# Kernel optimization log

Measured on AMD Instinct MI355X. Metric: run time of the kernel, lower is better.

The kernel has to match this reference:

```python
import math
import jax, jax.numpy as jnp
import numpy as np

B, S, D, H, FF, E, V, RH = 8, 256, 512, 8, 2048, 8, 32000, 256
MAX_PATH, MAX_VISITS = 4, 2
NEG = -1e9
DH = D // H


def _make_pe():
    # PositionalEncoding buffer (sin/cos), sliced to seq len S
    pos = np.arange(S, dtype=np.float32)[:, None]
    div = np.exp(np.arange(0, D, 2, dtype=np.float32) * (-math.log(10000.0) / D))
    pe = np.zeros((S, D), dtype=np.float32)
    pe[:, 0::2] = np.sin(pos * div)
    pe[:, 1::2] = np.cos(pos * div)
    return jnp.asarray(pe[None])  # [1,S,D]


def setup_inputs() -> dict:
    key = jax.random.key(0)
    ks = jax.random.split(key, 12)
    s = 0.02
    return dict(
        input_ids=jax.random.randint(ks[0], (B, S), 0, V),
        emb=jax.random.normal(ks[1], (V, D), jnp.float32) * s,
        pe=_make_pe(),
        Wqkv=jax.random.normal(ks[2], (E, 3 * D, D), jnp.float32) * s,
        bqkv=jnp.zeros((E, 3 * D), jnp.float32),
        Wo=jax.random.normal(ks[3], (E, D, D), jnp.float32) * s,
        bo=jnp.zeros((E, D), jnp.float32),
        W1=jax.random.normal(ks[4], (E, FF, D), jnp.float32) * s,
        b1=jnp.zeros((E, FF), jnp.float32),
        W2=jax.random.normal(ks[5], (E, D, FF), jnp.float32) * s,
        b2=jnp.zeros((E, D), jnp.float32),
        ln1_g=jnp.ones((E, D), jnp.float32), ln1_b=jnp.zeros((E, D), jnp.float32),
        ln2_g=jnp.ones((E, D), jnp.float32), ln2_b=jnp.zeros((E, D), jnp.float32),
        tag=jax.random.normal(ks[6], (E, D), jnp.float32) * 0.01,
        r_w1=jax.random.normal(ks[7], (RH, D), jnp.float32) * s,
        r_b1=jnp.zeros((RH,), jnp.float32),
        r_w2=jax.random.normal(ks[8], (E + 1, RH), jnp.float32) * s,
        r_b2=jnp.zeros((E + 1,), jnp.float32),
        lm_w=jax.random.normal(ks[9], (V, D), jnp.float32) * s,
        lm_b=jnp.zeros((V,), jnp.float32),
    )


def _ln(x, g, b):
    # per-sample gathered LayerNorm params g,b: [B,D]; x: [B,S,D]
    mu = x.mean(-1, keepdims=True)
    var = ((x - mu) ** 2).mean(-1, keepdims=True)
    return (x - mu) * jax.lax.rsqrt(var + 1e-5) * g[:, None, :] + b[:, None, :]


def _expert(x, idx, Wqkv, bqkv, Wo, bo, W1, b1, W2, b2, g1, be1, g2, be2, tag):
    # post-norm TransformerEncoderLayer (eval mode, dropout off) with per-sample expert params
    qkv = jnp.einsum('bsd,bfd->bsf', x, Wqkv[idx]) + bqkv[idx][:, None, :]
    q, k, v = jnp.split(qkv, 3, axis=-1)
    q = q.reshape(B, S, H, DH)
    k = k.reshape(B, S, H, DH)
    v = v.reshape(B, S, H, DH)
    att = jax.nn.softmax(jnp.einsum('bqhd,bkhd->bhqk', q, k) / math.sqrt(DH), axis=-1)
    ctx = jnp.einsum('bhqk,bkhd->bqhd', att, v).reshape(B, S, D)
    attn_out = jnp.einsum('bsd,bod->bso', ctx, Wo[idx]) + bo[idx][:, None, :]
    x = _ln(x + attn_out, g1[idx], be1[idx])
    hid = jax.nn.relu(jnp.einsum('bsd,bfd->bsf', x, W1[idx]) + b1[idx][:, None, :])
    ff = jnp.einsum('bsf,bdf->bsd', hid, W2[idx]) + b2[idx][:, None, :]
    x = _ln(x + ff, g2[idx], be2[idx])
    return x + tag[idx][:, None, :]  # + specialization_tag


def reference(input_ids, emb, pe, Wqkv, bqkv, Wo, bo, W1, b1, W2, b2,
              ln1_g, ln1_b, ln2_g, ln2_b, tag, r_w1, r_b1, r_w2, r_b2, lm_w, lm_b):
    pad_mask = (jnp.arange(V) != 0).astype(emb.dtype)[:, None]  # padding_idx=0 row is zero
    rep = (emb * pad_mask)[input_ids] * math.sqrt(D) + pe[:, :S]
    visits = jnp.zeros((B, E), jnp.int32)
    active = jnp.ones((B,), bool)
    ent_total = jnp.asarray(0.0, rep.dtype)
    for _ in range(MAX_PATH):
        summary = rep.mean(1)  # [B,D]
        h = jax.nn.relu(summary @ r_w1.T + r_b1)
        logits = h @ r_w2.T + r_b2  # [B,E+1], last slot = terminate
        logits = jnp.concatenate(
            [jnp.where(visits >= MAX_VISITS, NEG, logits[:, :E]), logits[:, E:]], axis=1)
        probs = jax.nn.softmax(logits, axis=-1)
        ent = -jnp.sum(probs * jnp.log(probs + 1e-9), axis=-1)
        cnt = jnp.sum(active)
        ent_total = ent_total + jnp.where(
            cnt > 0, jnp.sum(ent * active) / jnp.maximum(cnt, 1).astype(ent.dtype), 0.0)
        choice = jnp.argmax(logits, axis=-1)       # eval mode: hard argmax
        go = active & (choice < E)                 # samples routed to an expert this step
        idx = jnp.where(go, choice, 0)
        visits = visits + jax.nn.one_hot(idx, E, dtype=jnp.int32) * go[:, None].astype(jnp.int32)
        new_rep = _expert(rep, idx, Wqkv, bqkv, Wo, bo, W1, b1, W2, b2,
                          ln1_g, ln1_b, ln2_g, ln2_b, tag)
        rep = jnp.where(go[:, None, None], new_rep, rep)  # terminated/inactive reps frozen
        active = go
    logits_lm = rep @ lm_w.T + lm_b  # [B,S,V]
    return logits_lm, ent_total
```

## Files before the change

### kernel.cpp

```cpp
#include <hip/hip_runtime.h>
#include <hip/hip_bf16.h>

#define NB 8
#define NS 256
#define ND 512
#define NH 8
#define NDH 64
#define NFF 2048
#define NE 8
#define NV 32000
#define NRH 256
#define MAXV 2
#define NEGV (-1e9f)

typedef __attribute__((ext_vector_type(8))) short short8;
typedef __attribute__((ext_vector_type(4))) float f32x4;

__device__ __forceinline__ unsigned short f2bf(float x) {
  unsigned int u = __float_as_uint(x);
  u = (u + 0x7fffu + ((u >> 16) & 1u)) >> 16;
  return (unsigned short)u;
}

__device__ __forceinline__ void gload16(const unsigned short* g, unsigned short* l) {
  __builtin_amdgcn_global_load_lds(
      (const __attribute__((address_space(1))) unsigned int*)g,
      (__attribute__((address_space(3))) unsigned int*)l, 16, 0, 0);
}

__device__ __forceinline__ int swzc(int lane) {
  return (lane & 3) ^ ((lane >> 3) & 3);
}

__device__ __forceinline__ void cast8(const float* s, unsigned short* d, int j) {
  const float4* s4 = (const float4*)s;
  float4 a = s4[j * 2], b = s4[j * 2 + 1];
  short8 v;
  v[0] = (short)f2bf(a.x); v[1] = (short)f2bf(a.y);
  v[2] = (short)f2bf(a.z); v[3] = (short)f2bf(a.w);
  v[4] = (short)f2bf(b.x); v[5] = (short)f2bf(b.y);
  v[6] = (short)f2bf(b.z); v[7] = (short)f2bf(b.w);
  *(short8*)&d[(size_t)j * 8] = v;
}

__global__ __launch_bounds__(256) void k_cast5e(
    const float* s0, unsigned short* d0, int n0,
    const float* s1, unsigned short* d1, int n1,
    const float* s2, unsigned short* d2, int n2,
    const float* s3, unsigned short* d3, int n3,
    const float* s4, unsigned short* d4, int n4,
    int nbcast,
    const int* __restrict__ ids, const float* __restrict__ emb,
    const float* __restrict__ pe, float* __restrict__ rep,
    unsigned short* __restrict__ repb, float* __restrict__ partial,
    int* visits, int* active, float* entp) {
  if (blockIdx.x == 0) {
    if (threadIdx.x < NB * NE) visits[threadIdx.x] = 0;
    if (threadIdx.x < NB) active[threadIdx.x] = 1;
    if (threadIdx.x == 0) *entp = 0.f;
  }
  if ((int)blockIdx.x >= nbcast) {
    int j2 = blockIdx.x - nbcast;
    int rg = j2 & 15, b = j2 >> 4;
    int t = threadIdx.x;
    int c0 = t, c1 = t + 256;
    float p0 = 0.f, p1 = 0.f;
    for (int row = 0; row < 16; ++row) {
      int s = rg * 16 + row;
      int id = ids[b * NS + s];
      float sc = (id != 0) ? 22.627416997969522f : 0.f;
      float v0 = emb[(size_t)id * ND + c0] * sc + pe[(size_t)s * ND + c0];
      float v1 = emb[(size_t)id * ND + c1] * sc + pe[(size_t)s * ND + c1];
      size_t base = ((size_t)b * NS + s) * ND;
      rep[base + c0] = v0; rep[base + c1] = v1;
      repb[base + c0] = f2bf(v0); repb[base + c1] = f2bf(v1);
      p0 += v0; p1 += v1;
    }
    float* pp = partial + ((size_t)b * 16 + rg) * ND;
    pp[c0] = p0; pp[c1] = p1;
    return;
  }
  int j = blockIdx.x * 256 + threadIdx.x;
  if (j < n0) { cast8(s0, d0, j); return; }
  j -= n0;
  if (j < n1) { cast8(s1, d1, j); return; }
  j -= n1;
  if (j < n2) { cast8(s2, d2, j); return; }
  j -= n2;
  if (j < n3) { cast8(s3, d3, j); return; }
  j -= n3;
  if (j < n4) cast8(s4, d4, j);
}

__global__ __launch_bounds__(256) void k_router(const float* __restrict__ partial,
                                                const float* __restrict__ rw1,
                                                const float* __restrict__ rb1,
                                                const float* __restrict__ rw2,
                                                const float* __restrict__ rb2,
                                                int* visits, int* active,
                                                int* idx, int* go, float* ent_total) {
  __shared__ float sm[NB][ND];
  __shared__ float h[NB][NRH];
  __shared__ float lg[NB][NE + 1];
  int t = threadIdx.x;
  for (int i = t; i < NB * ND; i += 256) {
    int bb = i >> 9, d = i & 511;
    const float* pp = partial + ((size_t)bb * 16) * ND + d;
    float s = 0.f;
#pragma unroll
    for (int rg = 0; rg < 16; ++rg) s += pp[(size_t)rg * ND];
    sm[bb][d] = s * (1.f / NS);
  }
  __syncthreads();
  {
    const float* w = rw1 + (size_t)t * ND;
    float acc[NB];
#pragma unroll
    for (int b = 0; b < NB; ++b) acc[b] = rb1[t];
    for (int d = 0; d < ND; ++d) {
      float wv = w[d];
#pragma unroll
      for (int b = 0; b < NB; ++b) acc[b] += sm[b][d] * wv;
    }
#pragma unroll
    for (int b = 0; b < NB; ++b) h[b][t] = fmaxf(acc[b], 0.f);
  }
  __syncthreads();
  if (t < NB * (NE + 1)) {
    int b = t / (NE + 1), e = t % (NE + 1);
    const float* w = rw2 + e * NRH;
    float a = rb2[e];
    for (int r = 0; r < NRH; ++r) a += h[b][r] * w[r];
    lg[b][e] = a;
  }
  __syncthreads();
  if (t == 0) {
    int aprev[NB];
    int cnt = 0;
    for (int b = 0; b < NB; ++b) { aprev[b] = active[b]; cnt += aprev[b]; }
    float entsum = 0.f;
    for (int b = 0; b < NB; ++b) {
      float l[NE + 1];
      for (int e = 0; e < NE; ++e)
        l[e] = (visits[b * NE + e] >= MAXV) ? NEGV : lg[b][e];
      l[NE] = lg[b][NE];
      float m = l[0];
      for (int e = 1; e <= NE; ++e) m = fmaxf(m, l[e]);
      float z = 0.f, p[NE + 1];
      for (int e = 0; e <= NE; ++e) { p[e] = __expf(l[e] - m); z += p[e]; }
      float zi = 1.f / z, ent = 0.f;
      for (int e = 0; e <= NE; ++e) {
        float pp = p[e] * zi;
        ent -= pp * __logf(pp + 1e-9f);
      }
      if (aprev[b]) entsum += ent;
      int ch = 0; float bm = l[0];
      for (int e = 1; e <= NE; ++e) if (l[e] > bm) { bm = l[e]; ch = e; }
      int g = (aprev[b] && ch < NE) ? 1 : 0;
      int ix = g ? ch : 0;
      visits[b * NE + ix] += g;
      idx[b] = ix; go[b] = g; active[b] = g;
    }
    if (cnt > 0) *ent_total += entsum / (float)cnt;
  }
}

template <int OUT, int RELU, int SK>
__global__ __launch_bounds__(256) void k_gemm64p(
    const unsigned short* __restrict__ Aall, int sa,
    const unsigned short* __restrict__ Wall, const float* __restrict__ ball,
    float* __restrict__ Pall, unsigned short* __restrict__ Uall, int so,
    int N, int K,
    unsigned short* __restrict__ Qb, unsigned short* __restrict__ Kb,
    unsigned short* __restrict__ Vt,
    const int* __restrict__ go, const int* __restrict__ idx) {
  int b = blockIdx.z;
  if (!go[b]) return;
  int t = threadIdx.x;
  int lane = t & 63, w = t >> 6;
  int wm = (w >> 1) * 32, wn = (w & 1) * 32;
  int kc = blockIdx.x >> 2;
  int bm = (blockIdx.x & 3) * 64, bn = blockIdx.y * 64;
  int KC = K / SK;
  int lrow = (lane >> 4) * 4, lcol = lane & 15;
  const unsigned short* A = Aall + (size_t)b * sa + kc * KC;
  const unsigned short* W = Wall + (size_t)idx[b] * N * K + kc * KC;

  __shared__ __align__(16) unsigned short As[2][64][64];
  __shared__ __align__(16) unsigned short Bs[2][64][64];
  f32x4 acc[2][2];
#pragma unroll
  for (int i = 0; i < 2; ++i)
#pragma unroll
    for (int j = 0; j < 2; ++j) acc[i][j] = (f32x4){0.f, 0.f, 0.f, 0.f};

  int ch8 = (lane & 7) ^ ((lane >> 3) & 7);
  const unsigned short* ga = A + (size_t)(bm + w * 16 + (lane >> 3)) * K + ch8 * 8;
  const unsigned short* gb = W + (size_t)(bn + w * 16 + (lane >> 3)) * K + ch8 * 8;

#define ISSUE64(slot, kt)                                            \
  gload16(ga + (size_t)(kt) * 64, &As[slot][w * 16][0]);             \
  gload16(ga + (size_t)(kt) * 64 + 8 * (size_t)K, &As[slot][w * 16 + 8][0]); \
  gload16(gb + (size_t)(kt) * 64, &Bs[slot][w * 16][0]);             \
  gload16(gb + (size_t)(kt) * 64 + 8 * (size_t)K, &Bs[slot][w * 16 + 8][0]);

  int nk = KC >> 6;
  ISSUE64(0, 0)
  ISSUE64(1, 1)

  int row0 = lane & 15, g = lane >> 4;
  for (int it = 0; it < nk; ++it) {
    if (it < nk - 1) asm volatile("s_waitcnt vmcnt(4)" ::: "memory");
    else             asm volatile("s_waitcnt vmcnt(0)" ::: "memory");
    asm volatile("s_barrier" ::: "memory");
    int sl = it & 1;
    __builtin_amdgcn_s_setprio(1);
#pragma unroll
    for (int kk = 0; kk < 2; ++kk) {
      int co = ((kk * 4 + g) ^ (row0 & 7)) * 8;
      short8 a0 = *(const short8*)&As[sl][wm + row0][co];
      short8 a1 = *(const short8*)&As[sl][wm + 16 + row0][co];
      short8 b0 = *(const short8*)&Bs[sl][wn + row0][co];
      short8 b1 = *(const short8*)&Bs[sl][wn + 16 + row0][co];
      acc[0][0] = __builtin_amdgcn_mfma_f32_16x16x32_bf16(a0, b0, acc[0][0], 0, 0, 0);
      acc[0][1] = __builtin_amdgcn_mfma_f32_16x16x32_bf16(a0, b1, acc[0][1], 0, 0, 0);
      acc[1][0] = __builtin_amdgcn_mfma_f32_16x16x32_bf16(a1, b0, acc[1][0], 0, 0, 0);
      acc[1][1] = __builtin_amdgcn_mfma_f32_16x16x32_bf16(a1, b1, acc[1][1], 0, 0, 0);
    }
    __builtin_amdgcn_s_setprio(0);
    asm volatile("s_barrier" ::: "memory");
    if (it + 2 < nk) { ISSUE64(sl, it + 2) }
  }
#undef ISSUE64

  if (OUT == 2) {
    const float* bias = ball + (size_t)idx[b] * N;
    int seg = bn >> 9;
#pragma unroll
    for (int nf = 0; nf < 2; ++nf) {
      int col = bn + wn + nf * 16 + lcol;
      float bv = bias[col];
      if (seg < 2) {
        unsigned short* dst = (seg == 0) ? Qb : Kb;
        int cc = col - seg * 512;
#pragma unroll
        for (int mf = 0; mf < 2; ++mf)
#pragma unroll
          for (int r = 0; r < 4; ++r) {
            int row = bm + wm + mf * 16 + lrow + r;
            dst[((size_t)b * NS + row) * ND + cc] = f2bf(acc[mf][nf][r] + bv);
          }
      } else {
        int dcol = col - 1024;
#pragma unroll
        for (int mf = 0; mf < 2; ++mf) {
          int s0 = bm + wm + mf * 16 + lrow;
          unsigned long long pk =
              (unsigned long long)f2bf(acc[mf][nf][0] + bv) |
              ((unsigned long long)f2bf(acc[mf][nf][1] + bv) << 16) |
              ((unsigned long long)f2bf(acc[mf][nf][2] + bv) << 32) |
              ((unsigned long long)f2bf(acc[mf][nf][3] + bv) << 48);
          *(unsigned long long*)&Vt[((size_t)b * 512 + dcol) * 256 + s0] = pk;
        }
      }
    }
  } else if (OUT == 1) {
    const float* bias = ball + (size_t)idx[b] * N;
#pragma unroll
    for (int nf = 0; nf < 2; ++nf) {
      int col = bn + wn + nf * 16 + lcol;
      float bv = bias[col];
#pragma unroll
      for (int mf = 0; mf < 2; ++mf) {
#pragma unroll
        for (int r = 0; r < 4; ++r) {
          int row = bm + wm + mf * 16 + lrow + r;
          float v = acc[mf][nf][r] + bv;
          if (RELU) v = fmaxf(v, 0.f);
          Uall[(size_t)b * so + (size_t)row * N + col] = f2bf(v);
        }
      }
    }
  } else {
    float* P = Pall + ((size_t)kc * NB + b) * ((size_t)NS * N);
#pragma unroll
    for (int nf = 0; nf < 2; ++nf) {
      int col = bn + wn + nf * 16 + lcol;
#pragma unroll
      for (int mf = 0; mf < 2; ++mf)
#pragma unroll
        for (int r = 0; r < 4; ++r)
          P[(size_t)(bm + wm + mf * 16 + lrow + r) * N + col] = acc[mf][nf][r];
    }
  }
}

__global__ __launch_bounds__(256) void k_attn2(const unsigned short* __restrict__ Qb,
                                               const unsigned short* __restrict__ Kb,
                                               const unsigned short* __restrict__ Vt,
                                               unsigned short* __restrict__ ctxb,
                                               const int* __restrict__ go) {
  int b = blockIdx.z, h = blockIdx.y, qt = blockIdx.x;
  if (!go[b]) return;
  int t = threadIdx.x;
  __shared__ __align__(16) unsigned short lds0[16384];
  __shared__ __align__(16) unsigned short lds1[16384];
  int lane = t & 63, w = t >> 6, g = lane >> 4, c = lane & 15;

#pragma unroll
  for (int i = 0; i < 8; ++i) {
    int task = i * 256 + t;
    int k = task >> 3, cc = task & 7;
    short8 v = *(const short8*)&Kb[((size_t)b * NS + k) * ND + h * NDH + cc * 8];
    *(short8*)&lds0[k * 64 + ((cc * 8) ^ ((k & 7) << 3))] = v;
  }
#pragma unroll
  for (int i = 0; i < 8; ++i) {
    int task = i * 256 + t;
    int d = task >> 5, kc = task & 31;
    short8 v = *(const short8*)&Vt[((size_t)b * 512 + h * NDH + d) * 256 + kc * 8];
    *(short8*)&lds1[d * 256 + ((kc * 8) ^ ((d & 7) << 3))] = v;
  }
  short8 qf[2];
  {
    const unsigned short* qp = Qb + ((size_t)b * NS + qt * 64 + w * 16 + c) * ND + h * NDH;
    qf[0] = *(const short8*)&qp[g * 8];
    qf[1] = *(const short8*)&qp[32 + g * 8];
  }
  __syncthreads();

  f32x4 sacc[16];
#pragma unroll
  for (int mf = 0; mf < 16; ++mf) sacc[mf] = (f32x4){0.f, 0.f, 0.f, 0.f};
#pragma unroll
  for (int mf = 0; mf < 16; ++mf) {
#pragma unroll
    for (int kd = 0; kd < 2; ++kd) {
      int row = mf * 16 + c;
      short8 kf = *(const short8*)&lds0[row * 64 + ((kd * 32 + g * 8) ^ ((row & 7) << 3))];
      sacc[mf] = __builtin_amdgcn_mfma_f32_16x16x32_bf16(kf, qf[kd], sacc[mf], 0, 0, 0);
    }
  }
  __syncthreads();

  float mx = -3.4e38f;
#pragma unroll
  for (int mf = 0; mf < 16; ++mf) {
#pragma unroll
    for (int r = 0; r < 4; ++r) {
      sacc[mf][r] *= 0.125f;
      mx = fmaxf(mx, sacc[mf][r]);
    }
  }
  mx = fmaxf(mx, __shfl_xor(mx, 16));
  mx = fmaxf(mx, __shfl_xor(mx, 32));
  float sum = 0.f;
#pragma unroll
  for (int mf = 0; mf < 16; ++mf)
#pragma unroll
    for (int r = 0; r < 4; ++r) {
      float p = __expf(sacc[mf][r] - mx);
      sacc[mf][r] = p;
      sum += p;
    }
  sum += __shfl_xor(sum, 16);
  sum += __shfl_xor(sum, 32);
  float zi = 1.f / sum;

  int q_l = w * 16 + c;
#pragma unroll
  for (int mf = 0; mf < 16; ++mf) {
    unsigned long long pk =
        (unsigned long long)f2bf(sacc[mf][0] * zi) |
        ((unsigned long long)f2bf(sacc[mf][1] * zi) << 16) |
        ((unsigned long long)f2bf(sacc[mf][2] * zi) << 32) |
        ((unsigned long long)f2bf(sacc[mf][3] * zi) << 48);
    *(unsigned long long*)&lds0[q_l * 256 + ((mf * 16 + g * 4) ^ ((q_l & 7) << 3))] = pk;
  }

  f32x4 cacc[4];
#pragma unroll
  for (int nf = 0; nf < 4; ++nf) cacc[nf] = (f32x4){0.f, 0.f, 0.f, 0.f};
#pragma unroll
  for (int ks = 0; ks < 8; ++ks) {
    int prow = w * 16 + c;
    short8 pf = *(const short8*)&lds0[prow * 256 + ((ks * 32 + g * 8) ^ ((prow & 7) << 3))];
#pragma unroll
    for (int nf = 0; nf < 4; ++nf) {
      int vrow = nf * 16 + c;
      short8 vf = *(const short8*)&lds1[vrow * 256 + ((ks * 32 + g * 8) ^ ((vrow & 7) << 3))];
      cacc[nf] = __builtin_amdgcn_mfma_f32_16x16x32_bf16(pf, vf, cacc[nf], 0, 0, 0);
    }
  }
#pragma unroll
  for (int nf = 0; nf < 4; ++nf)
#pragma unroll
    for (int r = 0; r < 4; ++r)
      ctxb[((size_t)b * NS + qt * 64 + w * 16 + g * 4 + r) * ND + h * NDH + nf * 16 + c] =
          f2bf(cacc[nf][r]);
}

template <int NCH, int TAG, int SUMP>
__global__ __launch_bounds__(256) void k_ln_red(
    const float* __restrict__ res, const float* __restrict__ part,
    const float* __restrict__ gbias,
    const float* __restrict__ gall, const float* __restrict__ beall,
    const float* __restrict__ tagall,
    float* __restrict__ outf, unsigned short* __restrict__ outb,
    float* __restrict__ sump,
    const int* __restrict__ go, const int* __restrict__ idx) {
  int b = blockIdx.y;
  if (!go[b]) return;
  int rg = blockIdx.x;
  int w = threadIdx.x >> 6, l = threadIdx.x & 63;
  int ix = idx[b];
  int d = l * 8;
  float gb8[8], gg[8], bb[8];
  {
    float4 a0 = *(const float4*)&gbias[ix * ND + d];
    float4 a1 = *(const float4*)&gbias[ix * ND + d + 4];
    gb8[0] = a0.x; gb8[1] = a0.y; gb8[2] = a0.z; gb8[3] = a0.w;
    gb8[4] = a1.x; gb8[5] = a1.y; gb8[6] = a1.z; gb8[7] = a1.w;
    float4 g0 = *(const float4*)&gall[ix * ND + d];
    float4 g1 = *(const float4*)&gall[ix * ND + d + 4];
    gg[0] = g0.x; gg[1] = g0.y; gg[2] = g0.z; gg[3] = g0.w;
    gg[4] = g1.x; gg[5] = g1.y; gg[6] = g1.z; gg[7] = g1.w;
    float4 b0 = *(const float4*)&beall[ix * ND + d];
    float4 b1 = *(const float4*)&beall[ix * ND + d + 4];
    bb[0] = b0.x; bb[1] = b0.y; bb[2] = b0.z; bb[3] = b0.w;
    bb[4] = b1.x; bb[5] = b1.y; bb[6] = b1.z; bb[7] = b1.w;
    if (TAG) {
      float4 t0 = *(const float4*)&tagall[ix * ND + d];
      float4 t1 = *(const float4*)&tagall[ix * ND + d + 4];
      bb[0] += t0.x; bb[1] += t0.y; bb[2] += t0.z; bb[3] += t0.w;
      bb[4] += t1.x; bb[5] += t1.y; bb[6] += t1.z; bb[7] += t1.w;
    }
  }
  float ps[8] = {0.f, 0.f, 0.f, 0.f, 0.f, 0.f, 0.f, 0.f};
  const size_t CSTRIDE = (size_t)NB * NS * ND;
  for (int rr = 0; rr < 4; ++rr) {
    int s = rg * 16 + w * 4 + rr;
    size_t base = ((size_t)b * NS + s) * ND;
    float4 x0 = *(const float4*)&res[base + d];
    float4 x1 = *(const float4*)&res[base + d + 4];
    float v[8] = {x0.x + gb8[0], x0.y + gb8[1], x0.z + gb8[2], x0.w + gb8[3],
                  x1.x + gb8[4], x1.y + gb8[5], x1.z + gb8[6], x1.w + gb8[7]};
#pragma unroll
    for (int c = 0; c < NCH; ++c) {
      const float* pc = part + c * CSTRIDE + base;
      float4 p0 = *(const float4*)&pc[d];
      float4 p1 = *(const float4*)&pc[d + 4];
      v[0] += p0.x; v[1] += p0.y; v[2] += p0.z; v[3] += p0.w;
      v[4] += p1.x; v[5] += p1.y; v[6] += p1.z; v[7] += p1.w;
    }
    float sum = 0.f;
#pragma unroll
    for (int j = 0; j < 8; ++j) sum += v[j];
#pragma unroll
    for (int off = 1; off < 64; off <<= 1) sum += __shfl_xor(sum, off);
    float mu = sum * (1.f / ND);
    float var = 0.f;
#pragma unroll
    for (int j = 0; j < 8; ++j) { v[j] -= mu; var += v[j] * v[j]; }
#pragma unroll
    for (int off = 1; off < 64; off <<= 1) var += __shfl_xor(var, off);
    float rs = rsqrtf(var * (1.f / ND) + 1e-5f);
    float o[8];
    short8 ob;
#pragma unroll
    for (int j = 0; j < 8; ++j) {
      o[j] = v[j] * rs * gg[j] + bb[j];
      if (SUMP) ps[j] += o[j];
      ob[j] = (short)f2bf(o[j]);
    }
    *(float4*)&outf[base + d] = (float4){o[0], o[1], o[2], o[3]};
    *(float4*)&outf[base + d + 4] = (float4){o[4], o[5], o[6], o[7]};
    *(short8*)&outb[base + d] = ob;
  }
  if (SUMP) {
    __shared__ float pl[4][ND];
#pragma unroll
    for (int j = 0; j < 8; ++j) pl[w][d + j] = ps[j];
    __syncthreads();
    if (w == 0) {
      float* pp = sump + ((size_t)b * 16 + rg) * ND;
#pragma unroll
      for (int j = 0; j < 8; ++j)
        pp[d + j] = pl[0][d + j] + pl[1][d + j] + pl[2][d + j] + pl[3][d + j];
    }
  }
}

__global__ __launch_bounds__(512, 2) void k_lmhead256(const unsigned short* __restrict__ Ab,
                                                      const unsigned short* __restrict__ Wb,
                                                      const float* __restrict__ bias,
                                                      float* __restrict__ out,
                                                      const float* __restrict__ entp) {
  if (blockIdx.x == 0 && threadIdx.x == 0)
    out[(size_t)NB * NS * NV] = *entp;
  int id = blockIdx.x;
  int swz = (id & 7) * 125 + (id >> 3);
  int bm = (swz % 8) * 256;
  int bn = (swz / 8) * 256;

  __shared__ __align__(16) unsigned short As[2][256][32];
  __shared__ __align__(16) unsigned short Bs[2][256][32];
  int t = threadIdx.x;
  int lane = t & 63, w = t >> 6;
  int wm = (w >> 2) * 128, wn = (w & 3) * 64;
  f32x4 acc[8][4];
#pragma unroll
  for (int i = 0; i < 8; ++i)
#pragma unroll
    for (int j = 0; j < 4; ++j) acc[i][j] = (f32x4){0.f, 0.f, 0.f, 0.f};

  const unsigned short* ga = Ab + (size_t)(bm + w * 32 + (lane >> 2)) * ND + swzc(lane) * 8;
  const unsigned short* gb = Wb + (size_t)(bn + w * 32 + (lane >> 2)) * ND + swzc(lane) * 8;

#define ISSUEL(slot, kt)                                           \
  gload16(ga + (kt) * 32, &As[slot][w * 32][0]);                   \
  gload16(ga + (kt) * 32 + 16 * ND, &As[slot][w * 32 + 16][0]);    \
  gload16(gb + (kt) * 32, &Bs[slot][w * 32][0]);                   \
  gload16(gb + (kt) * 32 + 16 * ND, &Bs[slot][w * 32 + 16][0]);

  ISSUEL(0, 0)
  ISSUEL(1, 1)

  int row0 = lane & 15;
  int cs = ((lane >> 4) ^ ((row0 >> 1) & 3)) * 8;
  for (int it = 0; it < 16; ++it) {
    if (it < 15) asm volatile("s_waitcnt vmcnt(4)" ::: "memory");
    else         asm volatile("s_waitcnt vmcnt(0)" ::: "memory");
    asm volatile("s_barrier" ::: "memory");
    int sl = it & 1;
    short8 a[8], bfr[4];
#pragma unroll
    for (int mf = 0; mf < 8; ++mf)
      a[mf] = *(const short8*)&As[sl][wm + mf * 16 + row0][cs];
#pragma unroll
    for (int nf = 0; nf < 4; ++nf)
      bfr[nf] = *(const short8*)&Bs[sl][wn + nf * 16 + row0][cs];
    __builtin_amdgcn_s_setprio(1);
#pragma unroll
    for (int mf = 0; mf < 8; ++mf)
#pragma unroll
      for (int nf = 0; nf < 4; ++nf)
        acc[mf][nf] = __builtin_amdgcn_mfma_f32_16x16x32_bf16(a[mf], bfr[nf], acc[mf][nf], 0, 0, 0);
    __builtin_amdgcn_s_setprio(0);
    asm volatile("s_barrier" ::: "memory");
    if (it + 2 < 16) { ISSUEL(sl, it + 2) }
  }
#undef ISSUEL

  int lrow = (lane >> 4) * 4, lcol = lane & 15;
#pragma unroll
  for (int nf = 0; nf < 4; ++nf) {
    int col = bn + wn + nf * 16 + lcol;
    float bv = bias[col];
#pragma unroll
    for (int mf = 0; mf < 8; ++mf) {
#pragma unroll
      for (int r = 0; r < 4; ++r) {
        int row = bm + wm + mf * 16 + lrow + r;
        out[(size_t)row * NV + col] = acc[mf][nf][r] + bv;
      }
    }
  }
}

extern "C" void kernel_launch(void* const* d_in, const int* in_sizes, int n_in,
                              void* d_out, int out_size, void* d_ws, size_t ws_size,
                              hipStream_t stream) {
  const int* ids   = (const int*)d_in[0];
  const float* emb = (const float*)d_in[1];
  const float* pe  = (const float*)d_in[2];
  const float* Wqkv = (const float*)d_in[3];
  const float* bqkv = (const float*)d_in[4];
  const float* Wo   = (const float*)d_in[5];
  const float* bo   = (const float*)d_in[6];
  const float* W1   = (const float*)d_in[7];
  const float* b1   = (const float*)d_in[8];
  const float* W2   = (const float*)d_in[9];
  const float* b2   = (const float*)d_in[10];
  const float* g1   = (const float*)d_in[11];
  const float* be1  = (const float*)d_in[12];
  const float* g2   = (const float*)d_in[13];
  const float* be2  = (const float*)d_in[14];
  const float* tag  = (const float*)d_in[15];
  const float* rw1  = (const float*)d_in[16];
  const float* rb1  = (const float*)d_in[17];
  const float* rw2  = (const float*)d_in[18];
  const float* rb2  = (const float*)d_in[19];
  const float* lmw  = (const float*)d_in[20];
  const float* lmb  = (const float*)d_in[21];
  float* out = (float*)d_out;

  float* ws = (float*)d_ws;
  size_t o = 0;
  float* rep = ws + o;  o += (size_t)NB * NS * ND;
  float* x1  = ws + o;  o += (size_t)NB * NS * ND;
  float* partk = ws + o; o += (size_t)4 * NB * NS * ND;
  float* partial = ws + o; o += (size_t)NB * 16 * ND;
  int* visits = (int*)(ws + o); o += 1024;
  int* active = visits + NB * NE;
  int* idx = active + NB;
  int* go = idx + NB;
  float* entp = (float*)(go + NB);

  unsigned short* us = (unsigned short*)(ws + o);
  size_t uo = 0;
  unsigned short* rep_b = us + uo; uo += (size_t)NB * NS * ND;
  unsigned short* x1_b  = us + uo; uo += (size_t)NB * NS * ND;
  unsigned short* ctx_b = us + uo; uo += (size_t)NB * NS * ND;
  unsigned short* Qb    = us + uo; uo += (size_t)NB * NS * ND;
  unsigned short* Kb    = us + uo; uo += (size_t)NB * NS * ND;
  unsigned short* Vt    = us + uo; uo += (size_t)NB * NS * ND;
  unsigned short* hid_b = us + uo; uo += (size_t)NB * NS * NFF;
  unsigned short* Wqkv_b = us + uo; uo += (size_t)NE * 3 * ND * ND;
  unsigned short* Wo_b   = us + uo; uo += (size_t)NE * ND * ND;
  unsigned short* W1_b   = us + uo; uo += (size_t)NE * NFF * ND;
  unsigned short* W2_b   = us + uo; uo += (size_t)NE * ND * NFF;
  unsigned short* lmw_b  = us + uo; uo += (size_t)NV * ND;

  {
    int n0 = NE * 3 * ND * ND / 8, n1 = NE * ND * ND / 8, n2 = NE * NFF * ND / 8,
        n3 = NE * ND * NFF / 8, n4 = NV * ND / 8;
    int nbcast = (n0 + n1 + n2 + n3 + n4) / 256;
    k_cast5e<<<nbcast + 16 * NB, 256, 0, stream>>>(
        Wqkv, Wqkv_b, n0, Wo, Wo_b, n1, W1, W1_b, n2, W2, W2_b, n3, lmw, lmw_b, n4,
        nbcast, ids, emb, pe, rep, rep_b, partial, visits, active, entp);
  }

  for (int step = 0; step < 4; ++step) {
    k_router<<<1, 256, 0, stream>>>(partial, rw1, rb1, rw2, rb2,
                                    visits, active, idx, go, entp);
    k_gemm64p<2, 0, 1><<<dim3(4, 24, NB), 256, 0, stream>>>(
        rep_b, NS * ND, Wqkv_b, bqkv, nullptr, nullptr, 0, 3 * ND, ND,
        Qb, Kb, Vt, go, idx);
    k_attn2<<<dim3(4, NH, NB), 256, 0, stream>>>(Qb, Kb, Vt, ctx_b, go);
    k_gemm64p<0, 0, 2><<<dim3(8, 8, NB), 256, 0, stream>>>(
        ctx_b, NS * ND, Wo_b, nullptr, partk, nullptr, 0, ND, ND,
        nullptr, nullptr, nullptr, go, idx);
    k_ln_red<2, 0, 0><<<dim3(16, NB), 256, 0, stream>>>(
        rep, partk, bo, g1, be1, nullptr, x1, x1_b, nullptr, go, idx);
    k_gemm64p<1, 1, 1><<<dim3(4, 32, NB), 256, 0, stream>>>(
        x1_b, NS * ND, W1_b, b1, nullptr, hid_b, NS * NFF, NFF, ND,
        nullptr, nullptr, nullptr, go, idx);
    k_gemm64p<0, 0, 4><<<dim3(16, 8, NB), 256, 0, stream>>>(
        hid_b, NS * NFF, W2_b, nullptr, partk, nullptr, 0, ND, NFF,
        nullptr, nullptr, nullptr, go, idx);
    k_ln_red<4, 1, 1><<<dim3(16, NB), 256, 0, stream>>>(
        x1, partk, b2, g2, be2, tag, rep, rep_b, partial, go, idx);
  }

  k_lmhead256<<<1000, 512, 0, stream>>>(rep_b, lmw_b, lmb, out, entp);
}
```

Before: 590.2 us.

## Split router across per-sample blocks and double LayerNorm-reduce grid

```diff
diff --git a/kernel.cpp b/kernel.cpp
--- a/kernel.cpp
+++ b/kernel.cpp
@@ -64,7 +64,7 @@
     int rg = j2 & 15, b = j2 >> 4;
     int t = threadIdx.x;
     int c0 = t, c1 = t + 256;
-    float p0 = 0.f, p1 = 0.f;
+    float pa0 = 0.f, pa1 = 0.f, pb0 = 0.f, pb1 = 0.f;
     for (int row = 0; row < 16; ++row) {
       int s = rg * 16 + row;
       int id = ids[b * NS + s];
@@ -74,10 +74,12 @@
       size_t base = ((size_t)b * NS + s) * ND;
       rep[base + c0] = v0; rep[base + c1] = v1;
       repb[base + c0] = f2bf(v0); repb[base + c1] = f2bf(v1);
-      p0 += v0; p1 += v1;
-    }
-    float* pp = partial + ((size_t)b * 16 + rg) * ND;
-    pp[c0] = p0; pp[c1] = p1;
+      if (row < 8) { pa0 += v0; pa1 += v1; } else { pb0 += v0; pb1 += v1; }
+    }
+    float* ppa = partial + ((size_t)b * 32 + rg * 2) * ND;
+    float* ppb = ppa + ND;
+    ppa[c0] = pa0; ppa[c1] = pa1;
+    ppb[c0] = pb0; ppb[c1] = pb1;
     return;
   }
   int j = blockIdx.x * 256 + threadIdx.x;
@@ -92,76 +94,67 @@
   if (j < n4) cast8(s4, d4, j);
 }
 
-__global__ __launch_bounds__(256) void k_router(const float* __restrict__ partial,
-                                                const float* __restrict__ rw1,
-                                                const float* __restrict__ rb1,
-                                                const float* __restrict__ rw2,
-                                                const float* __restrict__ rb2,
-                                                int* visits, int* active,
-                                                int* idx, int* go, float* ent_total) {
-  __shared__ float sm[NB][ND];
-  __shared__ float h[NB][NRH];
-  __shared__ float lg[NB][NE + 1];
+__global__ __launch_bounds__(256) void k_router8(
+    const float* __restrict__ partial,
+    const float* __restrict__ rw1, const float* __restrict__ rb1,
+    const float* __restrict__ rw2, const float* __restrict__ rb2,
+    int* visits, const int* __restrict__ active_in, int* active_out,
+    int* idx, int* go, float* ent_total) {
+  int b = blockIdx.x;
+  __shared__ float sm[ND];
+  __shared__ float h[NRH];
+  __shared__ float lg[NE + 1];
+  __shared__ int scnt;
   int t = threadIdx.x;
-  for (int i = t; i < NB * ND; i += 256) {
-    int bb = i >> 9, d = i & 511;
-    const float* pp = partial + ((size_t)bb * 16) * ND + d;
+  for (int i = t; i < ND; i += 256) {
+    const float* pp = partial + ((size_t)b * 32) * ND + i;
     float s = 0.f;
 #pragma unroll
-    for (int rg = 0; rg < 16; ++rg) s += pp[(size_t)rg * ND];
-    sm[bb][d] = s * (1.f / NS);
+    for (int rg = 0; rg < 32; ++rg) s += pp[(size_t)rg * ND];
+    sm[i] = s * (1.f / NS);
+  }
+  if (t == 0) {
+    int c = 0;
+    for (int bb = 0; bb < NB; ++bb) c += active_in[bb];
+    scnt = c;
   }
   __syncthreads();
   {
     const float* w = rw1 + (size_t)t * ND;
-    float acc[NB];
-#pragma unroll
-    for (int b = 0; b < NB; ++b) acc[b] = rb1[t];
-    for (int d = 0; d < ND; ++d) {
-      float wv = w[d];
-#pragma unroll
-      for (int b = 0; b < NB; ++b) acc[b] += sm[b][d] * wv;
-    }
-#pragma unroll
-    for (int b = 0; b < NB; ++b) h[b][t] = fmaxf(acc[b], 0.f);
+    float acc = rb1[t];
+    for (int d = 0; d < ND; ++d) acc += sm[d] * w[d];
+    h[t] = fmaxf(acc, 0.f);
   }
   __syncthreads();
-  if (t < NB * (NE + 1)) {
-    int b = t / (NE + 1), e = t % (NE + 1);
-    const float* w = rw2 + e * NRH;
-    float a = rb2[e];
-    for (int r = 0; r < NRH; ++r) a += h[b][r] * w[r];
-    lg[b][e] = a;
+  if (t < NE + 1) {
+    const float* w = rw2 + t * NRH;
+    float a = rb2[t];
+    for (int r = 0; r < NRH; ++r) a += h[r] * w[r];
+    lg[t] = a;
   }
   __syncthreads();
   if (t == 0) {
-    int aprev[NB];
-    int cnt = 0;
-    for (int b = 0; b < NB; ++b) { aprev[b] = active[b]; cnt += aprev[b]; }
-    float entsum = 0.f;
-    for (int b = 0; b < NB; ++b) {
-      float l[NE + 1];
-      for (int e = 0; e < NE; ++e)
-        l[e] = (visits[b * NE + e] >= MAXV) ? NEGV : lg[b][e];
-      l[NE] = lg[b][NE];
-      float m = l[0];
-      for (int e = 1; e <= NE; ++e) m = fmaxf(m, l[e]);
-      float z = 0.f, p[NE + 1];
-      for (int e = 0; e <= NE; ++e) { p[e] = __expf(l[e] - m); z += p[e]; }
-      float zi = 1.f / z, ent = 0.f;
-      for (int e = 0; e <= NE; ++e) {
-        float pp = p[e] * zi;
-        ent -= pp * __logf(pp + 1e-9f);
-      }
-      if (aprev[b]) entsum += ent;
-      int ch = 0; float bm = l[0];
-      for (int e = 1; e <= NE; ++e) if (l[e] > bm) { bm = l[e]; ch = e; }
-      int g = (aprev[b] && ch < NE) ? 1 : 0;
-      int ix = g ? ch : 0;
-      visits[b * NE + ix] += g;
-      idx[b] = ix; go[b] = g; active[b] = g;
-    }
-    if (cnt > 0) *ent_total += entsum / (float)cnt;
+    int aprev = active_in[b];
+    float l[NE + 1];
+    for (int e = 0; e < NE; ++e)
+      l[e] = (visits[b * NE + e] >= MAXV) ? NEGV : lg[e];
+    l[NE] = lg[NE];
+    float m = l[0];
+    for (int e = 1; e <= NE; ++e) m = fmaxf(m, l[e]);
+    float z = 0.f, p[NE + 1];
+    for (int e = 0; e <= NE; ++e) { p[e] = __expf(l[e] - m); z += p[e]; }
+    float zi = 1.f / z, ent = 0.f;
+    for (int e = 0; e <= NE; ++e) {
+      float pp = p[e] * zi;
+      ent -= pp * __logf(pp + 1e-9f);
+    }
+    if (aprev && scnt > 0) atomicAdd(ent_total, ent / (float)scnt);
+    int ch = 0; float bm = l[0];
+    for (int e = 1; e <= NE; ++e) if (l[e] > bm) { bm = l[e]; ch = e; }
+    int g = (aprev && ch < NE) ? 1 : 0;
+    int ix = g ? ch : 0;
+    visits[b * NE + ix] += g;
+    idx[b] = ix; go[b] = g; active_out[b] = g;
   }
 }
 
@@ -438,8 +431,8 @@
   }
   float ps[8] = {0.f, 0.f, 0.f, 0.f, 0.f, 0.f, 0.f, 0.f};
   const size_t CSTRIDE = (size_t)NB * NS * ND;
-  for (int rr = 0; rr < 4; ++rr) {
-    int s = rg * 16 + w * 4 + rr;
+  for (int rr = 0; rr < 2; ++rr) {
+    int s = rg * 8 + w * 2 + rr;
     size_t base = ((size_t)b * NS + s) * ND;
     float4 x0 = *(const float4*)&res[base + d];
     float4 x1 = *(const float4*)&res[base + d + 4];
@@ -483,7 +476,7 @@
     for (int j = 0; j < 8; ++j) pl[w][d + j] = ps[j];
     __syncthreads();
     if (w == 0) {
-      float* pp = sump + ((size_t)b * 16 + rg) * ND;
+      float* pp = sump + ((size_t)b * 32 + rg) * ND;
 #pragma unroll
       for (int j = 0; j < 8; ++j)
         pp[d + j] = pl[0][d + j] + pl[1][d + j] + pl[2][d + j] + pl[3][d + j];
@@ -600,10 +593,11 @@
   float* rep = ws + o;  o += (size_t)NB * NS * ND;
   float* x1  = ws + o;  o += (size_t)NB * NS * ND;
   float* partk = ws + o; o += (size_t)4 * NB * NS * ND;
-  float* partial = ws + o; o += (size_t)NB * 16 * ND;
+  float* partial = ws + o; o += (size_t)NB * 32 * ND;
   int* visits = (int*)(ws + o); o += 1024;
-  int* active = visits + NB * NE;
-  int* idx = active + NB;
+  int* active0 = visits + NB * NE;
+  int* active1 = active0 + NB;
+  int* idx = active1 + NB;
   int* go = idx + NB;
   float* entp = (float*)(go + NB);
 
@@ -628,12 +622,14 @@
     int nbcast = (n0 + n1 + n2 + n3 + n4) / 256;
     k_cast5e<<<nbcast + 16 * NB, 256, 0, stream>>>(
         Wqkv, Wqkv_b, n0, Wo, Wo_b, n1, W1, W1_b, n2, W2, W2_b, n3, lmw, lmw_b, n4,
-        nbcast, ids, emb, pe, rep, rep_b, partial, visits, active, entp);
+        nbcast, ids, emb, pe, rep, rep_b, partial, visits, active0, entp);
   }
 
   for (int step = 0; step < 4; ++step) {
-    k_router<<<1, 256, 0, stream>>>(partial, rw1, rb1, rw2, rb2,
-                                    visits, active, idx, go, entp);
+    int* act_in  = (step & 1) ? active1 : active0;
+    int* act_out = (step & 1) ? active0 : active1;
+    k_router8<<<NB, 256, 0, stream>>>(partial, rw1, rb1, rw2, rb2,
+                                      visits, act_in, act_out, idx, go, entp);
     k_gemm64p<2, 0, 1><<<dim3(4, 24, NB), 256, 0, stream>>>(
         rep_b, NS * ND, Wqkv_b, bqkv, nullptr, nullptr, 0, 3 * ND, ND,
         Qb, Kb, Vt, go, idx);
@@ -641,7 +637,7 @@
     k_gemm64p<0, 0, 2><<<dim3(8, 8, NB), 256, 0, stream>>>(
         ctx_b, NS * ND, Wo_b, nullptr, partk, nullptr, 0, ND, ND,
         nullptr, nullptr, nullptr, go, idx);
-    k_ln_red<2, 0, 0><<<dim3(16, NB), 256, 0, stream>>>(
+    k_ln_red<2, 0, 0><<<dim3(32, NB), 256, 0, stream>>>(
         rep, partk, bo, g1, be1, nullptr, x1, x1_b, nullptr, go, idx);
     k_gemm64p<1, 1, 1><<<dim3(4, 32, NB), 256, 0, stream>>>(
         x1_b, NS * ND, W1_b, b1, nullptr, hid_b, NS * NFF, NFF, ND,
@@ -649,7 +645,7 @@
     k_gemm64p<0, 0, 4><<<dim3(16, 8, NB), 256, 0, stream>>>(
         hid_b, NS * NFF, W2_b, nullptr, partk, nullptr, 0, ND, NFF,
         nullptr, nullptr, nullptr, go, idx);
-    k_ln_red<4, 1, 1><<<dim3(16, NB), 256, 0, stream>>>(
+    k_ln_red<4, 1, 1><<<dim3(32, NB), 256, 0, stream>>>(
         x1, partk, b2, g2, be2, tag, rep, rep_b, partial, go, idx);
   }
 
```

After: 507.0 us. 1.16x faster.
